# Kernel optimization log

Measured on AMD Instinct MI355X. Metric: run time of the kernel, lower is better.

The kernel has to match this reference:

```python
import jax, jax.numpy as jnp
import numpy as np

NS = 150            # number of MC weight samples
D_IN, D_H, D_OUT = 1024, 512, 256


def setup_inputs() -> dict:
    key = jax.random.key(0)
    ks = jax.random.split(key, 9)
    x = jax.random.normal(ks[0], (32, D_IN), dtype=jnp.float32)
    # variational means (mu network params)
    mu_W1 = jax.random.normal(ks[1], (D_H, D_IN), dtype=jnp.float32) * 0.02
    mu_b1 = jnp.zeros((D_H,), dtype=jnp.float32)
    mu_W2 = jax.random.normal(ks[2], (D_OUT, D_H), dtype=jnp.float32) * 0.02
    mu_b2 = jnp.zeros((D_OUT,), dtype=jnp.float32)
    # variational log-stds (std network params v); std = exp(v)
    v_W1 = -3.0 + 0.1 * jax.random.normal(ks[3], (D_H, D_IN), dtype=jnp.float32)
    v_b1 = -3.0 + 0.1 * jax.random.normal(ks[4], (D_H,), dtype=jnp.float32)
    v_W2 = -3.0 + 0.1 * jax.random.normal(ks[5], (D_OUT, D_H), dtype=jnp.float32)
    v_b2 = -3.0 + 0.1 * jax.random.normal(ks[6], (D_OUT,), dtype=jnp.float32)
    return {
        "x": x,
        "mu_W1": mu_W1, "mu_b1": mu_b1, "mu_W2": mu_W2, "mu_b2": mu_b2,
        "v_W1": v_W1, "v_b1": v_b1, "v_W2": v_W2, "v_b2": v_b2,
    }


def reference(x, mu_W1, mu_b1, mu_W2, mu_b2, v_W1, v_b1, v_W2, v_b2):
    # Reparameterization: w = mu + eps * sqrt(exp(2v)) = mu + eps * exp(v)
    nk = jax.random.split(jax.random.key(42), 4)
    eW1 = jax.random.normal(nk[0], (NS,) + mu_W1.shape, dtype=mu_W1.dtype)
    eb1 = jax.random.normal(nk[1], (NS,) + mu_b1.shape, dtype=mu_b1.dtype)
    eW2 = jax.random.normal(nk[2], (NS,) + mu_W2.shape, dtype=mu_W2.dtype)
    eb2 = jax.random.normal(nk[3], (NS,) + mu_b2.shape, dtype=mu_b2.dtype)

    W1 = mu_W1 + eW1 * jnp.exp(v_W1)          # [ns, H, I]
    b1 = mu_b1 + eb1 * jnp.exp(v_b1)          # [ns, H]
    W2 = mu_W2 + eW2 * jnp.exp(v_W2)          # [ns, O, H]
    b2 = mu_b2 + eb2 * jnp.exp(v_b2)          # [ns, O]

    # MLP forward, batched over the ns sample axis
    h = jax.nn.relu(jnp.einsum('bi,nhi->nbh', x, W1) + b1[:, None, :])  # [ns, B, H]
    y = jnp.einsum('nbh,noh->nbo', h, W2) + b2[:, None, :]              # [ns, B, O]
    return y  # stacked MC outputs, [ns, B, O]
```

## Files before the change

### kernel.cpp

```cpp
#include <hip/hip_runtime.h>
#include <stdint.h>

#define NS 150
#define D_IN 1024
#define D_H 512
#define D_OUT 256

typedef __bf16 bf16x8 __attribute__((ext_vector_type(8)));
typedef float f32x4 __attribute__((ext_vector_type(4)));

#define OFF_XF    0u
#define OFF_MS1T  16384u
#define OFF_MS2T  1064960u
#define OFF_B1S   1327104u
#define OFF_B2S   1403904u
#define OFF_HB    1442304u

#define SQ2 1.41421354f
#define CT0 (SQ2 * -0.000200214257f)
#define CT1 (SQ2 * 0.000100950558f)
#define CT2 (SQ2 * 0.00134934322f)
#define CT3 (SQ2 * -0.00367342844f)
#define CT4 (SQ2 * 0.00573950773f)
#define CT5 (SQ2 * -0.0076224613f)
#define CT6 (SQ2 * 0.00943887047f)
#define CT7 (SQ2 * 0.246640727f)
#define CM8 (SQ2 * 1.50140941f)

#define DSQ2 1.4142135623730951
#define DA  (-0.6931471805599453)
#define ZC3 ((float)(DSQ2 * -4.39150654e-06 * DA*DA*DA*DA*DA))
#define ZC4 ((float)(DSQ2 * 0.00021858087   * DA*DA*DA*DA))
#define ZC5 ((float)(DSQ2 * -0.00125372503  * DA*DA*DA))
#define ZC6 ((float)(DSQ2 * -0.00417768164  * DA*DA))
#define ZC7 ((float)(DSQ2 * 0.246640727     * DA))
#define ZC8 ((float)(DSQ2 * 1.50140941))
#define ZSHIFT 3.6067376022224085f
#define ZCUT  -7.213475204444817f

#define TT0 (SQ2 * -0.000200214257f)
#define TT1 (SQ2 * 0.000100950558f)
#define TT2 (SQ2 * 0.00134934322f)
#define TT3 (SQ2 * -0.00367342844f)
#define TT4 (SQ2 * 0.00573950773f)
#define TT5 (SQ2 * -0.0076224613f)
#define TT6 (SQ2 * 0.00943887047f)
#define TT7 (SQ2 * 1.00167406f)
#define TT8 (SQ2 * 2.83297682f)

#define ROTL32(x, r) __builtin_rotateleft32((x), (r))

__host__ __device__ __forceinline__ void threefry2x32(uint32_t k0, uint32_t k1,
                                                      uint32_t x0, uint32_t x1,
                                                      uint32_t& o0, uint32_t& o1) {
  uint32_t k2 = k0 ^ k1 ^ 0x1BD11BDAu;
  x0 += k0; x1 += k1;
#define TFR(r) { x0 += x1; x1 = ROTL32(x1, r); x1 ^= x0; }
  TFR(13) TFR(15) TFR(26) TFR(6)
  x0 += k1; x1 += k2 + 1u;
  TFR(17) TFR(29) TFR(16) TFR(24)
  x0 += k2; x1 += k0 + 2u;
  TFR(13) TFR(15) TFR(26) TFR(6)
  x0 += k0; x1 += k1 + 3u;
  TFR(17) TFR(29) TFR(16) TFR(24)
  x0 += k1; x1 += k2 + 4u;
  TFR(13) TFR(15) TFR(26) TFR(6)
  x0 += k2; x1 += k0 + 5u;
#undef TFR
  o0 = x0; o1 = x1;
}

__device__ __forceinline__ float tf_normal(uint32_t k0, uint32_t k1, uint32_t idx) {
  uint32_t o0, o1;
  threefry2x32(k0, k1, 0u, idx, o0, o1);
  uint32_t bits = o0 ^ o1;
  uint32_t fb = (bits >> 9) | 0x3F800000u;
  float m = __uint_as_float(fb);
  const float lo = -0.99999994f;
  float u = fmaxf(fmaf(m, 2.0f, -3.0f), lo);
  float t = fmaf(u, -u, 1.0f);
  float w = -0.69314718056f * __builtin_amdgcn_logf(t);
  float p;
  if (w < 5.0f) {
    float ww = w - 2.5f;
    p = SQ2 * 2.81022636e-08f;
    p = fmaf(p, ww, SQ2 * 3.43273939e-07f);
    p = fmaf(p, ww, SQ2 * -3.5233877e-06f);
    p = fmaf(p, ww, SQ2 * -4.39150654e-06f);
    p = fmaf(p, ww, SQ2 * 0.00021858087f);
    p = fmaf(p, ww, SQ2 * -0.00125372503f);
    p = fmaf(p, ww, SQ2 * -0.00417768164f);
    p = fmaf(p, ww, SQ2 * 0.246640727f);
    p = fmaf(p, ww, SQ2 * 1.50140941f);
  } else {
    float ww = __builtin_amdgcn_sqrtf(w) - 3.0f;
    p = TT0;
    p = fmaf(p, ww, TT1); p = fmaf(p, ww, TT2); p = fmaf(p, ww, TT3);
    p = fmaf(p, ww, TT4); p = fmaf(p, ww, TT5); p = fmaf(p, ww, TT6);
    p = fmaf(p, ww, TT7); p = fmaf(p, ww, TT8);
  }
  return p * u;
}

#define TF_ADD8 \
  "v_add_u32 %[a0], %[a0], %[b0]\n\t" "v_add_u32 %[a1], %[a1], %[b1]\n\t" \
  "v_add_u32 %[a2], %[a2], %[b2]\n\t" "v_add_u32 %[a3], %[a3], %[b3]\n\t" \
  "v_add_u32 %[a4], %[a4], %[b4]\n\t" "v_add_u32 %[a5], %[a5], %[b5]\n\t" \
  "v_add_u32 %[a6], %[a6], %[b6]\n\t" "v_add_u32 %[a7], %[a7], %[b7]\n\t"
#define TF_ROT8(sh) \
  "v_alignbit_b32 %[b0], %[b0], %[b0], " sh "\n\t" \
  "v_alignbit_b32 %[b1], %[b1], %[b1], " sh "\n\t" \
  "v_alignbit_b32 %[b2], %[b2], %[b2], " sh "\n\t" \
  "v_alignbit_b32 %[b3], %[b3], %[b3], " sh "\n\t" \
  "v_alignbit_b32 %[b4], %[b4], %[b4], " sh "\n\t" \
  "v_alignbit_b32 %[b5], %[b5], %[b5], " sh "\n\t" \
  "v_alignbit_b32 %[b6], %[b6], %[b6], " sh "\n\t" \
  "v_alignbit_b32 %[b7], %[b7], %[b7], " sh "\n\t"
#define TF_XOR8 \
  "v_xor_b32 %[b0], %[b0], %[a0]\n\t" "v_xor_b32 %[b1], %[b1], %[a1]\n\t" \
  "v_xor_b32 %[b2], %[b2], %[a2]\n\t" "v_xor_b32 %[b3], %[b3], %[a3]\n\t" \
  "v_xor_b32 %[b4], %[b4], %[a4]\n\t" "v_xor_b32 %[b5], %[b5], %[a5]\n\t" \
  "v_xor_b32 %[b6], %[b6], %[a6]\n\t" "v_xor_b32 %[b7], %[b7], %[a7]\n\t"
#define TF_ROUND(sh) TF_ADD8 TF_ROT8(sh) TF_XOR8
#define TF_INJ(KA, KB) \
  "v_add_u32 %[a0], " KA ", %[a0]\n\t" "v_add_u32 %[a1], " KA ", %[a1]\n\t" \
  "v_add_u32 %[a2], " KA ", %[a2]\n\t" "v_add_u32 %[a3], " KA ", %[a3]\n\t" \
  "v_add_u32 %[a4], " KA ", %[a4]\n\t" "v_add_u32 %[a5], " KA ", %[a5]\n\t" \
  "v_add_u32 %[a6], " KA ", %[a6]\n\t" "v_add_u32 %[a7], " KA ", %[a7]\n\t" \
  "v_add_u32 %[b0], " KB ", %[b0]\n\t" "v_add_u32 %[b1], " KB ", %[b1]\n\t" \
  "v_add_u32 %[b2], " KB ", %[b2]\n\t" "v_add_u32 %[b3], " KB ", %[b3]\n\t" \
  "v_add_u32 %[b4], " KB ", %[b4]\n\t" "v_add_u32 %[b5], " KB ", %[b5]\n\t" \
  "v_add_u32 %[b6], " KB ", %[b6]\n\t" "v_add_u32 %[b7], " KB ", %[b7]\n\t"

__device__ __forceinline__ void tf8_bits(uint32_t k0, uint32_t k1, uint32_t k2,
                                         uint32_t idx0, uint32_t* bits) {
  uint32_t k2p1 = k2 + 1u, k0p2 = k0 + 2u, k1p3 = k1 + 3u;
  uint32_t k2p4 = k2 + 4u, k0p5 = k0 + 5u;
  uint32_t t0 = idx0 + k1;
  uint32_t a0 = k0, a1 = k0, a2 = k0, a3 = k0, a4 = k0, a5 = k0, a6 = k0, a7 = k0;
  uint32_t b0 = t0, b1 = t0 + 1u, b2 = t0 + 2u, b3 = t0 + 3u;
  uint32_t b4 = t0 + 4u, b5 = t0 + 5u, b6 = t0 + 6u, b7 = t0 + 7u;
  asm(TF_ROUND("19") TF_ROUND("17") TF_ROUND("6") TF_ROUND("26")
      TF_INJ("%[k1]", "%[k2p1]")
      TF_ROUND("15") TF_ROUND("3") TF_ROUND("16") TF_ROUND("8")
      TF_INJ("%[k2]", "%[k0p2]")
      TF_ROUND("19") TF_ROUND("17") TF_ROUND("6") TF_ROUND("26")
      TF_INJ("%[k0]", "%[k1p3]")
      TF_ROUND("15") TF_ROUND("3") TF_ROUND("16") TF_ROUND("8")
      TF_INJ("%[k1]", "%[k2p4]")
      TF_ROUND("19") TF_ROUND("17") TF_ROUND("6") TF_ROUND("26")
      TF_INJ("%[k2]", "%[k0p5]")
      : [a0]"+v"(a0), [a1]"+v"(a1), [a2]"+v"(a2), [a3]"+v"(a3),
        [a4]"+v"(a4), [a5]"+v"(a5), [a6]"+v"(a6), [a7]"+v"(a7),
        [b0]"+v"(b0), [b1]"+v"(b1), [b2]"+v"(b2), [b3]"+v"(b3),
        [b4]"+v"(b4), [b5]"+v"(b5), [b6]"+v"(b6), [b7]"+v"(b7)
      : [k0]"s"(k0), [k1]"s"(k1), [k2]"s"(k2), [k2p1]"s"(k2p1),
        [k0p2]"s"(k0p2), [k1p3]"s"(k1p3), [k2p4]"s"(k2p4), [k0p5]"s"(k0p5));
  bits[0] = a0 ^ b0; bits[1] = a1 ^ b1; bits[2] = a2 ^ b2; bits[3] = a3 ^ b3;
  bits[4] = a4 ^ b4; bits[5] = a5 ^ b5; bits[6] = a6 ^ b6; bits[7] = a7 ^ b7;
}

__device__ __forceinline__ float bits_normal(uint32_t bits) {
  uint32_t fb = (bits >> 9) | 0x3F800000u;
  float m = __uint_as_float(fb);
  const float lo = -0.99999994f;
  float u = fmaxf(fmaf(m, 2.0f, -3.0f), lo);
  float t = fmaf(u, -u, 1.0f);
  float z = __builtin_amdgcn_logf(t);
  float p;
  if (z > ZCUT) {
    float zz = z + ZSHIFT;
    p = ZC3;
    p = fmaf(p, zz, ZC4); p = fmaf(p, zz, ZC5); p = fmaf(p, zz, ZC6);
    p = fmaf(p, zz, ZC7); p = fmaf(p, zz, ZC8);
  } else {
    float w = -0.69314718056f * z;
    float ww = __builtin_amdgcn_sqrtf(w) - 3.0f;
    p = TT0;
    p = fmaf(p, ww, TT1); p = fmaf(p, ww, TT2); p = fmaf(p, ww, TT3);
    p = fmaf(p, ww, TT4); p = fmaf(p, ww, TT5); p = fmaf(p, ww, TT6);
    p = fmaf(p, ww, TT7); p = fmaf(p, ww, TT8);
  }
  return p * u;
}

__global__ __launch_bounds__(256) void prep_kernel(
    const float* __restrict__ x,
    const float* __restrict__ muW1, const float* __restrict__ vW1,
    const float* __restrict__ muW2, const float* __restrict__ vW2,
    const float* __restrict__ mub1, const float* __restrict__ vb1,
    const float* __restrict__ mub2, const float* __restrict__ vb2,
    float* __restrict__ ws,
    uint32_t kb1_0, uint32_t kb1_1, uint32_t kb2_0, uint32_t kb2_1) {
  int bb = blockIdx.x;
  int tid = threadIdx.x;
  if (bb < 2048) {
    int t = bb * 256 + tid;
    ((float2*)(ws + OFF_MS1T))[t] = make_float2(muW1[t], expf(vW1[t]));
  } else if (bb < 2560) {
    int t = (bb - 2048) * 256 + tid;
    ((float2*)(ws + OFF_MS2T))[t] = make_float2(muW2[t], expf(vW2[t]));
  } else if (bb < 2688) {
    int t = (bb - 2560) * 256 + tid;
    int j = t & 7, lane = (t >> 3) & 63, fidx = t >> 9;
    int s = fidx >> 1, f = fidx & 1;
    int b = f * 16 + (lane & 15);
    int k = s * 32 + ((lane >> 4) << 3) + j;
    ((__bf16*)(ws + OFF_XF))[t] = (__bf16)x[b * D_IN + k];
  } else if (bb < 2988) {
    int t = (bb - 2688) * 256 + tid;
    int h = t & 511;
    float eps = tf_normal(kb1_0, kb1_1, (uint32_t)t);
    ws[OFF_B1S + t] = fmaf(eps, expf(vb1[h]), mub1[h]);
  } else {
    int t = (bb - 2988) * 256 + tid;
    int o = t & 255;
    float eps = tf_normal(kb2_0, kb2_1, (uint32_t)t);
    ws[OFF_B2S + t] = fmaf(eps, expf(vb2[o]), mub2[o]);
  }
}

__global__ __launch_bounds__(256) void l1_kernel(
    const float* __restrict__ ws, uint32_t k0, uint32_t k1) {
  const float2* __restrict__ ms1 = (const float2*)(ws + OFF_MS1T);
  const bf16x8* __restrict__ xf = (const bf16x8*)(ws + OFF_XF);
  const float* __restrict__ b1s = ws + OFF_B1S;
  __bf16* __restrict__ hB = (__bf16*)(ws + OFF_HB);
  uint32_t k2 = k0 ^ k1 ^ 0x1BD11BDAu;

  __shared__ f32x4 lred[2][2][64];

  int lane = threadIdx.x & 63;
  int wib = threadIdx.x >> 6;
  int pairIdx = wib >> 1, khalf = wib & 1;
  int tile = blockIdx.x * 2 + pairIdx;
  int n = tile >> 5;
  int ht = tile & 31;
  int mrow = lane & 15, quad = lane >> 4;
  int h = ht * 16 + mrow;
  uint32_t base = ((uint32_t)(n * 512 + h)) << 10;
  const float2* __restrict__ msrow = ms1 + (size_t)h * D_IN;

  f32x4 acc0 = {0.f, 0.f, 0.f, 0.f}, acc1 = {0.f, 0.f, 0.f, 0.f};

  int send = khalf * 16 + 16;
  for (int s = khalf * 16; s < send; ++s) {
    int kq = s * 32 + quad * 8;
    const f32x4* msq = (const f32x4*)(msrow + kq);
    f32x4 q0 = msq[0], q1 = msq[1], q2 = msq[2], q3 = msq[3];
    bf16x8 b0 = xf[(s * 2 + 0) * 64 + lane];
    bf16x8 b1 = xf[(s * 2 + 1) * 64 + lane];
    uint32_t bits[8];
    tf8_bits(k0, k1, k2, base + (uint32_t)kq, bits);
    float mu[8], sd[8];
    mu[0]=q0[0]; sd[0]=q0[1]; mu[1]=q0[2]; sd[1]=q0[3];
    mu[2]=q1[0]; sd[2]=q1[1]; mu[3]=q1[2]; sd[3]=q1[3];
    mu[4]=q2[0]; sd[4]=q2[1]; mu[5]=q2[2]; sd[5]=q2[3];
    mu[6]=q3[0]; sd[6]=q3[1]; mu[7]=q3[2]; sd[7]=q3[3];
    bf16x8 a;
#pragma unroll
    for (int j = 0; j < 8; ++j) {
      float eps = bits_normal(bits[j]);
      a[j] = (__bf16)fmaf(eps, sd[j], mu[j]);
    }
    acc0 = __builtin_amdgcn_mfma_f32_16x16x32_bf16(a, b0, acc0, 0, 0, 0);
    acc1 = __builtin_amdgcn_mfma_f32_16x16x32_bf16(a, b1, acc1, 0, 0, 0);
  }

  if (khalf) {
    lred[pairIdx][0][lane] = acc0;
    lred[pairIdx][1][lane] = acc1;
  }
  __syncthreads();
  if (!khalf) {
    f32x4 r0 = lred[pairIdx][0][lane], r1 = lred[pairIdx][1][lane];
    acc0 += r0; acc1 += r1;
    int hq = ht * 16 + quad * 4;
    float4 bias = *(const float4*)(b1s + n * 512 + hq);
    float bv[4] = {bias.x, bias.y, bias.z, bias.w};
    union { __bf16 v[4]; uint2 u; } p0, p1;
#pragma unroll
    for (int r = 0; r < 4; ++r) {
      p0.v[r] = (__bf16)fmaxf(acc0[r] + bv[r], 0.0f);
      p1.v[r] = (__bf16)fmaxf(acc1[r] + bv[r], 0.0f);
    }
    *(uint2*)(hB + ((size_t)(n * 32 + mrow) * 512 + hq)) = p0.u;
    *(uint2*)(hB + ((size_t)(n * 32 + 16 + mrow) * 512 + hq)) = p1.u;
  }
}

__global__ __launch_bounds__(256) void l2_kernel(
    const float* __restrict__ ws, float* __restrict__ y,
    uint32_t k0, uint32_t k1) {
  const float2* __restrict__ ms2 = (const float2*)(ws + OFF_MS2T);
  const bf16x8* __restrict__ hB8 = (const bf16x8*)(ws + OFF_HB);
  const float* __restrict__ b2s = ws + OFF_B2S;
  uint32_t k2 = k0 ^ k1 ^ 0x1BD11BDAu;

  __shared__ f32x4 lred[2][2][64];

  int lane = threadIdx.x & 63;
  int wib = threadIdx.x >> 6;
  int pairIdx = wib >> 1, khalf = wib & 1;
  int tile = blockIdx.x * 2 + pairIdx;
  int n = tile >> 4;
  int ot = tile & 15;
  int mrow = lane & 15, quad = lane >> 4;
  int o = ot * 16 + mrow;
  uint32_t base = (uint32_t)(n * 256 + o) << 9;
  const float2* __restrict__ msrow = ms2 + (size_t)o * D_H;

  f32x4 acc0 = {0.f, 0.f, 0.f, 0.f}, acc1 = {0.f, 0.f, 0.f, 0.f};

  int send = khalf * 8 + 8;
  for (int s = khalf * 8; s < send; ++s) {
    int kq = s * 32 + quad * 8;
    const f32x4* msq = (const f32x4*)(msrow + kq);
    f32x4 q0 = msq[0], q1 = msq[1], q2 = msq[2], q3 = msq[3];
    bf16x8 b0 = hB8[(size_t)(n * 32 + mrow) * 64 + s * 4 + quad];
    bf16x8 b1 = hB8[(size_t)(n * 32 + 16 + mrow) * 64 + s * 4 + quad];
    uint32_t bits[8];
    tf8_bits(k0, k1, k2, base + (uint32_t)kq, bits);
    float mu[8], sd[8];
    mu[0]=q0[0]; sd[0]=q0[1]; mu[1]=q0[2]; sd[1]=q0[3];
    mu[2]=q1[0]; sd[2]=q1[1]; mu[3]=q1[2]; sd[3]=q1[3];
    mu[4]=q2[0]; sd[4]=q2[1]; mu[5]=q2[2]; sd[5]=q2[3];
    mu[6]=q3[0]; sd[6]=q3[1]; mu[7]=q3[2]; sd[7]=q3[3];
    bf16x8 a;
#pragma unroll
    for (int j = 0; j < 8; ++j) {
      float eps = bits_normal(bits[j]);
      a[j] = (__bf16)fmaf(eps, sd[j], mu[j]);
    }
    acc0 = __builtin_amdgcn_mfma_f32_16x16x32_bf16(a, b0, acc0, 0, 0, 0);
    acc1 = __builtin_amdgcn_mfma_f32_16x16x32_bf16(a, b1, acc1, 0, 0, 0);
  }

  if (khalf) {
    lred[pairIdx][0][lane] = acc0;
    lred[pairIdx][1][lane] = acc1;
  }
  __syncthreads();
  if (!khalf) {
    f32x4 r0 = lred[pairIdx][0][lane], r1 = lred[pairIdx][1][lane];
    acc0 += r0; acc1 += r1;
    int oq = ot * 16 + quad * 4;
    float4 bias = *(const float4*)(b2s + n * 256 + oq);
    float4 o0, o1;
    o0.x = acc0[0] + bias.x; o0.y = acc0[1] + bias.y;
    o0.z = acc0[2] + bias.z; o0.w = acc0[3] + bias.w;
    o1.x = acc1[0] + bias.x; o1.y = acc1[1] + bias.y;
    o1.z = acc1[2] + bias.z; o1.w = acc1[3] + bias.w;
    *(float4*)(y + (size_t)(n * 32 + mrow) * 256 + oq) = o0;
    *(float4*)(y + (size_t)(n * 32 + 16 + mrow) * 256 + oq) = o1;
  }
}

extern "C" void kernel_launch(void* const* d_in, const int* in_sizes, int n_in,
                              void* d_out, int out_size, void* d_ws, size_t ws_size,
                              hipStream_t stream) {
  const float* x = (const float*)d_in[0];
  const float* muW1 = (const float*)d_in[1];
  const float* mub1 = (const float*)d_in[2];
  const float* muW2 = (const float*)d_in[3];
  const float* mub2 = (const float*)d_in[4];
  const float* vW1 = (const float*)d_in[5];
  const float* vb1 = (const float*)d_in[6];
  const float* vW2 = (const float*)d_in[7];
  const float* vb2 = (const float*)d_in[8];
  float* y = (float*)d_out;
  float* ws = (float*)d_ws;

  uint32_t nk[4][2];
  for (uint32_t j = 0; j < 4; ++j) {
    threefry2x32(0u, 42u, 0u, j, nk[j][0], nk[j][1]);
  }

  prep_kernel<<<3138, 256, 0, stream>>>(
      x, muW1, vW1, muW2, vW2, mub1, vb1, mub2, vb2, ws,
      nk[1][0], nk[1][1], nk[3][0], nk[3][1]);

  l1_kernel<<<2400, 256, 0, stream>>>(ws, nk[0][0], nk[0][1]);

  l2_kernel<<<1200, 256, 0, stream>>>(ws, y, nk[2][0], nk[2][1]);
}
```

Before: 300.7 us.

## Fold Threefry key injections into add3, pack normal transform, shrink blocks

```diff
diff --git a/kernel.cpp b/kernel.cpp
--- a/kernel.cpp
+++ b/kernel.cpp
@@ -8,6 +8,7 @@
 
 typedef __bf16 bf16x8 __attribute__((ext_vector_type(8)));
 typedef float f32x4 __attribute__((ext_vector_type(4)));
+typedef float f32x2 __attribute__((ext_vector_type(2)));
 
 #define OFF_XF    0u
 #define OFF_MS1T  16384u
@@ -17,15 +18,6 @@
 #define OFF_HB    1442304u
 
 #define SQ2 1.41421354f
-#define CT0 (SQ2 * -0.000200214257f)
-#define CT1 (SQ2 * 0.000100950558f)
-#define CT2 (SQ2 * 0.00134934322f)
-#define CT3 (SQ2 * -0.00367342844f)
-#define CT4 (SQ2 * 0.00573950773f)
-#define CT5 (SQ2 * -0.0076224613f)
-#define CT6 (SQ2 * 0.00943887047f)
-#define CT7 (SQ2 * 0.246640727f)
-#define CM8 (SQ2 * 1.50140941f)
 
 #define DSQ2 1.4142135623730951
 #define DA  (-0.6931471805599453)
@@ -122,36 +114,53 @@
   "v_xor_b32 %[b4], %[b4], %[a4]\n\t" "v_xor_b32 %[b5], %[b5], %[a5]\n\t" \
   "v_xor_b32 %[b6], %[b6], %[a6]\n\t" "v_xor_b32 %[b7], %[b7], %[a7]\n\t"
 #define TF_ROUND(sh) TF_ADD8 TF_ROT8(sh) TF_XOR8
-#define TF_INJ(KA, KB) \
-  "v_add_u32 %[a0], " KA ", %[a0]\n\t" "v_add_u32 %[a1], " KA ", %[a1]\n\t" \
-  "v_add_u32 %[a2], " KA ", %[a2]\n\t" "v_add_u32 %[a3], " KA ", %[a3]\n\t" \
-  "v_add_u32 %[a4], " KA ", %[a4]\n\t" "v_add_u32 %[a5], " KA ", %[a5]\n\t" \
-  "v_add_u32 %[a6], " KA ", %[a6]\n\t" "v_add_u32 %[a7], " KA ", %[a7]\n\t" \
+#define TF_R1(sh) \
+  "v_add_u32 %[a0], %[k0], %[b0]\n\t" "v_add_u32 %[a1], %[k0], %[b1]\n\t" \
+  "v_add_u32 %[a2], %[k0], %[b2]\n\t" "v_add_u32 %[a3], %[k0], %[b3]\n\t" \
+  "v_add_u32 %[a4], %[k0], %[b4]\n\t" "v_add_u32 %[a5], %[k0], %[b5]\n\t" \
+  "v_add_u32 %[a6], %[k0], %[b6]\n\t" "v_add_u32 %[a7], %[k0], %[b7]\n\t" \
+  TF_ROT8(sh) TF_XOR8
+#define TF_BADD8(KB) \
   "v_add_u32 %[b0], " KB ", %[b0]\n\t" "v_add_u32 %[b1], " KB ", %[b1]\n\t" \
   "v_add_u32 %[b2], " KB ", %[b2]\n\t" "v_add_u32 %[b3], " KB ", %[b3]\n\t" \
   "v_add_u32 %[b4], " KB ", %[b4]\n\t" "v_add_u32 %[b5], " KB ", %[b5]\n\t" \
   "v_add_u32 %[b6], " KB ", %[b6]\n\t" "v_add_u32 %[b7], " KB ", %[b7]\n\t"
+#define TF_AADD8(KA) \
+  "v_add_u32 %[a0], " KA ", %[a0]\n\t" "v_add_u32 %[a1], " KA ", %[a1]\n\t" \
+  "v_add_u32 %[a2], " KA ", %[a2]\n\t" "v_add_u32 %[a3], " KA ", %[a3]\n\t" \
+  "v_add_u32 %[a4], " KA ", %[a4]\n\t" "v_add_u32 %[a5], " KA ", %[a5]\n\t" \
+  "v_add_u32 %[a6], " KA ", %[a6]\n\t" "v_add_u32 %[a7], " KA ", %[a7]\n\t"
+#define TF_A3F(KA) \
+  "v_add3_u32 %[a0], %[a0], %[b0], " KA "\n\t" \
+  "v_add3_u32 %[a1], %[a1], %[b1], " KA "\n\t" \
+  "v_add3_u32 %[a2], %[a2], %[b2], " KA "\n\t" \
+  "v_add3_u32 %[a3], %[a3], %[b3], " KA "\n\t" \
+  "v_add3_u32 %[a4], %[a4], %[b4], " KA "\n\t" \
+  "v_add3_u32 %[a5], %[a5], %[b5], " KA "\n\t" \
+  "v_add3_u32 %[a6], %[a6], %[b6], " KA "\n\t" \
+  "v_add3_u32 %[a7], %[a7], %[b7], " KA "\n\t"
+#define TF_RFOLD(KB, KA, sh) TF_BADD8(KB) TF_A3F(KA) TF_ROT8(sh) TF_XOR8
 
 __device__ __forceinline__ void tf8_bits(uint32_t k0, uint32_t k1, uint32_t k2,
                                          uint32_t idx0, uint32_t* bits) {
   uint32_t k2p1 = k2 + 1u, k0p2 = k0 + 2u, k1p3 = k1 + 3u;
   uint32_t k2p4 = k2 + 4u, k0p5 = k0 + 5u;
   uint32_t t0 = idx0 + k1;
-  uint32_t a0 = k0, a1 = k0, a2 = k0, a3 = k0, a4 = k0, a5 = k0, a6 = k0, a7 = k0;
+  uint32_t a0, a1, a2, a3, a4, a5, a6, a7;
   uint32_t b0 = t0, b1 = t0 + 1u, b2 = t0 + 2u, b3 = t0 + 3u;
   uint32_t b4 = t0 + 4u, b5 = t0 + 5u, b6 = t0 + 6u, b7 = t0 + 7u;
-  asm(TF_ROUND("19") TF_ROUND("17") TF_ROUND("6") TF_ROUND("26")
-      TF_INJ("%[k1]", "%[k2p1]")
-      TF_ROUND("15") TF_ROUND("3") TF_ROUND("16") TF_ROUND("8")
-      TF_INJ("%[k2]", "%[k0p2]")
-      TF_ROUND("19") TF_ROUND("17") TF_ROUND("6") TF_ROUND("26")
-      TF_INJ("%[k0]", "%[k1p3]")
-      TF_ROUND("15") TF_ROUND("3") TF_ROUND("16") TF_ROUND("8")
-      TF_INJ("%[k1]", "%[k2p4]")
-      TF_ROUND("19") TF_ROUND("17") TF_ROUND("6") TF_ROUND("26")
-      TF_INJ("%[k2]", "%[k0p5]")
-      : [a0]"+v"(a0), [a1]"+v"(a1), [a2]"+v"(a2), [a3]"+v"(a3),
-        [a4]"+v"(a4), [a5]"+v"(a5), [a6]"+v"(a6), [a7]"+v"(a7),
+  asm(TF_R1("19") TF_ROUND("17") TF_ROUND("6") TF_ROUND("26")
+      TF_RFOLD("%[k2p1]", "%[k1]", "15")
+      TF_ROUND("3") TF_ROUND("16") TF_ROUND("8")
+      TF_RFOLD("%[k0p2]", "%[k2]", "19")
+      TF_ROUND("17") TF_ROUND("6") TF_ROUND("26")
+      TF_RFOLD("%[k1p3]", "%[k0]", "15")
+      TF_ROUND("3") TF_ROUND("16") TF_ROUND("8")
+      TF_RFOLD("%[k2p4]", "%[k1]", "19")
+      TF_ROUND("17") TF_ROUND("6") TF_ROUND("26")
+      TF_AADD8("%[k2]") TF_BADD8("%[k0p5]")
+      : [a0]"=&v"(a0), [a1]"=&v"(a1), [a2]"=&v"(a2), [a3]"=&v"(a3),
+        [a4]"=&v"(a4), [a5]"=&v"(a5), [a6]"=&v"(a6), [a7]"=&v"(a7),
         [b0]"+v"(b0), [b1]"+v"(b1), [b2]"+v"(b2), [b3]"+v"(b3),
         [b4]"+v"(b4), [b5]"+v"(b5), [b6]"+v"(b6), [b7]"+v"(b7)
       : [k0]"s"(k0), [k1]"s"(k1), [k2]"s"(k2), [k2p1]"s"(k2p1),
@@ -160,28 +169,53 @@
   bits[4] = a4 ^ b4; bits[5] = a5 ^ b5; bits[6] = a6 ^ b6; bits[7] = a7 ^ b7;
 }
 
-__device__ __forceinline__ float bits_normal(uint32_t bits) {
-  uint32_t fb = (bits >> 9) | 0x3F800000u;
-  float m = __uint_as_float(fb);
-  const float lo = -0.99999994f;
-  float u = fmaxf(fmaf(m, 2.0f, -3.0f), lo);
-  float t = fmaf(u, -u, 1.0f);
-  float z = __builtin_amdgcn_logf(t);
-  float p;
-  if (z > ZCUT) {
-    float zz = z + ZSHIFT;
-    p = ZC3;
-    p = fmaf(p, zz, ZC4); p = fmaf(p, zz, ZC5); p = fmaf(p, zz, ZC6);
-    p = fmaf(p, zz, ZC7); p = fmaf(p, zz, ZC8);
-  } else {
-    float w = -0.69314718056f * z;
-    float ww = __builtin_amdgcn_sqrtf(w) - 3.0f;
-    p = TT0;
-    p = fmaf(p, ww, TT1); p = fmaf(p, ww, TT2); p = fmaf(p, ww, TT3);
-    p = fmaf(p, ww, TT4); p = fmaf(p, ww, TT5); p = fmaf(p, ww, TT6);
-    p = fmaf(p, ww, TT7); p = fmaf(p, ww, TT8);
-  }
+__device__ __forceinline__ float tail_eps(float z, float u) {
+  float w = -0.69314718056f * z;
+  float ww = __builtin_amdgcn_sqrtf(w) - 3.0f;
+  float p = TT0;
+  p = fmaf(p, ww, TT1); p = fmaf(p, ww, TT2); p = fmaf(p, ww, TT3);
+  p = fmaf(p, ww, TT4); p = fmaf(p, ww, TT5); p = fmaf(p, ww, TT6);
+  p = fmaf(p, ww, TT7); p = fmaf(p, ww, TT8);
   return p * u;
+}
+
+__device__ __forceinline__ bf16x8 gen_w8(uint32_t k0, uint32_t k1, uint32_t k2,
+                                         uint32_t ctr,
+                                         f32x4 q0, f32x4 q1, f32x4 q2, f32x4 q3) {
+  uint32_t bits[8];
+  tf8_bits(k0, k1, k2, ctr, bits);
+  float mu[8], sd[8];
+  mu[0]=q0[0]; sd[0]=q0[1]; mu[1]=q0[2]; sd[1]=q0[3];
+  mu[2]=q1[0]; sd[2]=q1[1]; mu[3]=q1[2]; sd[3]=q1[3];
+  mu[4]=q2[0]; sd[4]=q2[1]; mu[5]=q2[2]; sd[5]=q2[3];
+  mu[6]=q3[0]; sd[6]=q3[1]; mu[7]=q3[2]; sd[7]=q3[3];
+  bf16x8 a;
+#pragma unroll
+  for (int jp = 0; jp < 4; ++jp) {
+    int j0 = jp * 2, j1 = jp * 2 + 1;
+    f32x2 m;
+    m.x = __uint_as_float((bits[j0] >> 9) | 0x3F800000u);
+    m.y = __uint_as_float((bits[j1] >> 9) | 0x3F800000u);
+    f32x2 u = m * 2.0f - 3.0f;
+    u.x = fmaxf(u.x, -0.99999994f);
+    u.y = fmaxf(u.y, -0.99999994f);
+    f32x2 t = (-u) * u + 1.0f;
+    f32x2 z;
+    z.x = __builtin_amdgcn_logf(t.x);
+    z.y = __builtin_amdgcn_logf(t.y);
+    f32x2 zz = z + ZSHIFT;
+    f32x2 p = ZC3 * zz + ZC4;
+    p = p * zz + ZC5;
+    p = p * zz + ZC6;
+    p = p * zz + ZC7;
+    p = p * zz + ZC8;
+    f32x2 e = p * u;
+    if (z.x <= ZCUT) e.x = tail_eps(z.x, u.x);
+    if (z.y <= ZCUT) e.y = tail_eps(z.y, u.y);
+    a[j0] = (__bf16)fmaf(e.x, sd[j0], mu[j0]);
+    a[j1] = (__bf16)fmaf(e.y, sd[j1], mu[j1]);
+  }
+  return a;
 }
 
 __global__ __launch_bounds__(256) void prep_kernel(
@@ -220,7 +254,7 @@
   }
 }
 
-__global__ __launch_bounds__(256) void l1_kernel(
+__global__ __launch_bounds__(128) void l1_kernel(
     const float* __restrict__ ws, uint32_t k0, uint32_t k1) {
   const float2* __restrict__ ms1 = (const float2*)(ws + OFF_MS1T);
   const bf16x8* __restrict__ xf = (const bf16x8*)(ws + OFF_XF);
@@ -228,12 +262,11 @@
   __bf16* __restrict__ hB = (__bf16*)(ws + OFF_HB);
   uint32_t k2 = k0 ^ k1 ^ 0x1BD11BDAu;
 
-  __shared__ f32x4 lred[2][2][64];
+  __shared__ f32x4 lred[2][64];
 
   int lane = threadIdx.x & 63;
-  int wib = threadIdx.x >> 6;
-  int pairIdx = wib >> 1, khalf = wib & 1;
-  int tile = blockIdx.x * 2 + pairIdx;
+  int khalf = threadIdx.x >> 6;
+  int tile = blockIdx.x;
   int n = tile >> 5;
   int ht = tile & 31;
   int mrow = lane & 15, quad = lane >> 4;
@@ -250,30 +283,18 @@
     f32x4 q0 = msq[0], q1 = msq[1], q2 = msq[2], q3 = msq[3];
     bf16x8 b0 = xf[(s * 2 + 0) * 64 + lane];
     bf16x8 b1 = xf[(s * 2 + 1) * 64 + lane];
-    uint32_t bits[8];
-    tf8_bits(k0, k1, k2, base + (uint32_t)kq, bits);
-    float mu[8], sd[8];
-    mu[0]=q0[0]; sd[0]=q0[1]; mu[1]=q0[2]; sd[1]=q0[3];
-    mu[2]=q1[0]; sd[2]=q1[1]; mu[3]=q1[2]; sd[3]=q1[3];
-    mu[4]=q2[0]; sd[4]=q2[1]; mu[5]=q2[2]; sd[5]=q2[3];
-    mu[6]=q3[0]; sd[6]=q3[1]; mu[7]=q3[2]; sd[7]=q3[3];
-    bf16x8 a;
-#pragma unroll
-    for (int j = 0; j < 8; ++j) {
-      float eps = bits_normal(bits[j]);
-      a[j] = (__bf16)fmaf(eps, sd[j], mu[j]);
-    }
+    bf16x8 a = gen_w8(k0, k1, k2, base + (uint32_t)kq, q0, q1, q2, q3);
     acc0 = __builtin_amdgcn_mfma_f32_16x16x32_bf16(a, b0, acc0, 0, 0, 0);
     acc1 = __builtin_amdgcn_mfma_f32_16x16x32_bf16(a, b1, acc1, 0, 0, 0);
   }
 
   if (khalf) {
-    lred[pairIdx][0][lane] = acc0;
-    lred[pairIdx][1][lane] = acc1;
+    lred[0][lane] = acc0;
+    lred[1][lane] = acc1;
   }
   __syncthreads();
   if (!khalf) {
-    f32x4 r0 = lred[pairIdx][0][lane], r1 = lred[pairIdx][1][lane];
+    f32x4 r0 = lred[0][lane], r1 = lred[1][lane];
     acc0 += r0; acc1 += r1;
     int hq = ht * 16 + quad * 4;
     float4 bias = *(const float4*)(b1s + n * 512 + hq);
@@ -289,7 +310,7 @@
   }
 }
 
-__global__ __launch_bounds__(256) void l2_kernel(
+__global__ __launch_bounds__(128) void l2_kernel(
     const float* __restrict__ ws, float* __restrict__ y,
     uint32_t k0, uint32_t k1) {
   const float2* __restrict__ ms2 = (const float2*)(ws + OFF_MS2T);
@@ -297,12 +318,11 @@
   const float* __restrict__ b2s = ws + OFF_B2S;
   uint32_t k2 = k0 ^ k1 ^ 0x1BD11BDAu;
 
-  __shared__ f32x4 lred[2][2][64];
+  __shared__ f32x4 lred[2][64];
 
   int lane = threadIdx.x & 63;
-  int wib = threadIdx.x >> 6;
-  int pairIdx = wib >> 1, khalf = wib & 1;
-  int tile = blockIdx.x * 2 + pairIdx;
+  int khalf = threadIdx.x >> 6;
+  int tile = blockIdx.x;
   int n = tile >> 4;
   int ot = tile & 15;
   int mrow = lane & 15, quad = lane >> 4;
@@ -319,30 +339,18 @@
     f32x4 q0 = msq[0], q1 = msq[1], q2 = msq[2], q3 = msq[3];
     bf16x8 b0 = hB8[(size_t)(n * 32 + mrow) * 64 + s * 4 + quad];
     bf16x8 b1 = hB8[(size_t)(n * 32 + 16 + mrow) * 64 + s * 4 + quad];
-    uint32_t bits[8];
-    tf8_bits(k0, k1, k2, base + (uint32_t)kq, bits);
-    float mu[8], sd[8];
-    mu[0]=q0[0]; sd[0]=q0[1]; mu[1]=q0[2]; sd[1]=q0[3];
-    mu[2]=q1[0]; sd[2]=q1[1]; mu[3]=q1[2]; sd[3]=q1[3];
-    mu[4]=q2[0]; sd[4]=q2[1]; mu[5]=q2[2]; sd[5]=q2[3];
-    mu[6]=q3[0]; sd[6]=q3[1]; mu[7]=q3[2]; sd[7]=q3[3];
-    bf16x8 a;
-#pragma unroll
-    for (int j = 0; j < 8; ++j) {
-      float eps = bits_normal(bits[j]);
-      a[j] = (__bf16)fmaf(eps, sd[j], mu[j]);
-    }
+    bf16x8 a = gen_w8(k0, k1, k2, base + (uint32_t)kq, q0, q1, q2, q3);
     acc0 = __builtin_amdgcn_mfma_f32_16x16x32_bf16(a, b0, acc0, 0, 0, 0);
     acc1 = __builtin_amdgcn_mfma_f32_16x16x32_bf16(a, b1, acc1, 0, 0, 0);
   }
 
   if (khalf) {
-    lred[pairIdx][0][lane] = acc0;
-    lred[pairIdx][1][lane] = acc1;
+    lred[0][lane] = acc0;
+    lred[1][lane] = acc1;
   }
   __syncthreads();
   if (!khalf) {
-    f32x4 r0 = lred[pairIdx][0][lane], r1 = lred[pairIdx][1][lane];
+    f32x4 r0 = lred[0][lane], r1 = lred[1][lane];
     acc0 += r0; acc1 += r1;
     int oq = ot * 16 + quad * 4;
     float4 bias = *(const float4*)(b2s + n * 256 + oq);
@@ -380,7 +388,7 @@
       x, muW1, vW1, muW2, vW2, mub1, vb1, mub2, vb2, ws,
       nk[1][0], nk[1][1], nk[3][0], nk[3][1]);
 
-  l1_kernel<<<2400, 256, 0, stream>>>(ws, nk[0][0], nk[0][1]);
-
-  l2_kernel<<<1200, 256, 0, stream>>>(ws, y, nk[2][0], nk[2][1]);
-}
+  l1_kernel<<<4800, 128, 0, stream>>>(ws, nk[0][0], nk[0][1]);
+
+  l2_kernel<<<2400, 128, 0, stream>>>(ws, y, nk[2][0], nk[2][1]);
+}
```

New measurement: 316.2 us. 1.05x slower.
